# Optimization experiments

Measured on AMD Instinct MI355X. Metric: run time of the kernel, lower is better.

Reference implementation:

```python
import jax, jax.numpy as jnp
import numpy as np

N_NODES, N_EDGES, N_GRAPHS = 20000, 320000, 8
IN_CH, OUT_CH = 16, 64


def gat_conv(x, src, dst, W, a_src, a_dst, bias, heads, ch, concat):
    # PyG-style GATConv: linear -> per-edge attention logits -> edge softmax over dst -> scatter-sum
    n = x.shape[0]
    h = (x @ W).reshape(n, heads, ch)                      # [N,H,C]
    alpha_src = jnp.einsum('nhc,hc->nh', h, a_src)          # [N,H]
    alpha_dst = jnp.einsum('nhc,hc->nh', h, a_dst)
    e = jax.nn.leaky_relu(alpha_src[src] + alpha_dst[dst], 0.2)  # [E,H]
    emax = jax.ops.segment_max(e, dst, num_segments=n)      # safe: self-loops guarantee coverage
    ee = jnp.exp(e - emax[dst])
    denom = jax.ops.segment_sum(ee, dst, num_segments=n)
    alpha = ee / denom[dst]                                 # [E,H]
    msg = h[src] * alpha[:, :, None]                        # [E,H,C]
    out = jax.ops.segment_sum(msg, dst, num_segments=n)     # [N,H,C]
    out = out.reshape(n, heads * ch) if concat else out.mean(axis=1)
    return out + bias


def setup_inputs() -> dict:
    key = jax.random.key(0)
    ks = jax.random.split(key, 32)
    d = {}
    d['x'] = jax.random.normal(ks[0], (N_NODES, IN_CH), dtype=jnp.float32)
    d['edge_index'] = jax.random.randint(ks[1], (2, N_EDGES), 0, N_NODES)
    d['function_idx'] = jax.random.randint(ks[2], (8000,), 0, N_NODES)
    d['flag'] = jnp.sort(jax.random.randint(ks[3], (8000,), 0, N_GRAPHS))
    d['decision_var_idxes'] = jax.random.randint(ks[4], (N_GRAPHS,), 0, N_NODES)
    s = 0.1
    # conv1: in 16 -> 8 heads x 8
    d['W1'] = jax.random.normal(ks[5], (IN_CH, 64)) * s
    d['a_src1'] = jax.random.normal(ks[6], (8, 8)) * s
    d['a_dst1'] = jax.random.normal(ks[7], (8, 8)) * s
    d['b1'] = jnp.zeros((64,), jnp.float32)
    # conv2, conv3: 64 -> 8 heads x 8
    d['W2'] = jax.random.normal(ks[8], (64, 64)) * s
    d['a_src2'] = jax.random.normal(ks[9], (8, 8)) * s
    d['a_dst2'] = jax.random.normal(ks[10], (8, 8)) * s
    d['b2'] = jnp.zeros((64,), jnp.float32)
    d['W3'] = jax.random.normal(ks[11], (64, 64)) * s
    d['a_src3'] = jax.random.normal(ks[12], (8, 8)) * s
    d['a_dst3'] = jax.random.normal(ks[13], (8, 8)) * s
    d['b3'] = jnp.zeros((64,), jnp.float32)
    # conv4: 64 -> 4 heads x 64, concat=False (mean over heads)
    d['W4'] = jax.random.normal(ks[14], (64, 4 * OUT_CH)) * s
    d['a_src4'] = jax.random.normal(ks[15], (4, OUT_CH)) * s
    d['a_dst4'] = jax.random.normal(ks[16], (4, OUT_CH)) * s
    d['b4'] = jnp.zeros((OUT_CH,), jnp.float32)
    d['Wp'] = jax.random.normal(ks[17], (OUT_CH, OUT_CH)) * s
    d['Wt'] = jax.random.normal(ks[18], (OUT_CH, OUT_CH)) * s
    d['Wo'] = jax.random.normal(ks[19], (2 * OUT_CH, 1)) * s
    d['bo'] = jnp.zeros((1,), jnp.float32)
    return d


def reference(x, edge_index, function_idx, flag, decision_var_idxes,
              W1, a_src1, a_dst1, b1, W2, a_src2, a_dst2, b2,
              W3, a_src3, a_dst3, b3, W4, a_src4, a_dst4, b4,
              Wp, Wt, Wo, bo):
    n = x.shape[0]
    loops = jnp.arange(n)
    src = jnp.concatenate([edge_index[0], loops])
    dst = jnp.concatenate([edge_index[1], loops])
    h = jax.nn.elu(gat_conv(x, src, dst, W1, a_src1, a_dst1, b1, 8, 8, True))
    h = jax.nn.elu(gat_conv(h, src, dst, W2, a_src2, a_dst2, b2, 8, 8, True))
    h = jax.nn.elu(gat_conv(h, src, dst, W3, a_src3, a_dst3, b3, 8, 8, True))
    h = jax.nn.elu(gat_conv(h, src, dst, W4, a_src4, a_dst4, b4, 4, OUT_CH, False))
    # per-graph sum-pool over function nodes
    fp = jax.ops.segment_sum(h[function_idx], flag, num_segments=N_GRAPHS)  # [B,64]
    fp = fp @ Wp
    tgt = h[decision_var_idxes] @ Wt                                        # [B,64]
    z = jax.nn.elu(jnp.concatenate([fp, tgt], axis=1))                      # [B,128]
    return z @ Wo + bo                                                      # [B,1]
```

## Files before the change

### kernel.cpp

```cpp
#include <hip/hip_runtime.h>
#include <hip/hip_bf16.h>
#include <math.h>

typedef __hip_bfloat16 bf16;
typedef unsigned short u16;
typedef __attribute__((ext_vector_type(8))) short bf16x8;
typedef __attribute__((ext_vector_type(4))) float f32x4;

#define DEG_CAP 96

__device__ __forceinline__ float b2f(bf16 v){ return __bfloat162float(v); }
__device__ __forceinline__ u16 f2bu(float f){
  bf16 h = __float2bfloat16(f);
  return *reinterpret_cast<u16*>(&h);
}
__device__ __forceinline__ float bu2f(u16 u){
  bf16 h = *reinterpret_cast<bf16*>(&u);
  return __bfloat162float(h);
}
__device__ __forceinline__ float eluf(float x){ return x > 0.f ? x : __expf(x) - 1.f; }
__device__ __forceinline__ float lrelu(float x){ return x > 0.f ? x : 0.2f * x; }
__device__ __forceinline__ float ldr(const void* p, int i, int f){
  return f ? ((const float*)p)[i] : b2f(((const bf16*)p)[i]);
}

#define DPP_F(x, ctrl) __int_as_float(__builtin_amdgcn_update_dpp(0, __float_as_int(x), (ctrl), 0xF, 0xF, true))
__device__ __forceinline__ float dpp_max8(float x){
  x = fmaxf(x, DPP_F(x, 0xB1));
  x = fmaxf(x, DPP_F(x, 0x4E));
  x = fmaxf(x, DPP_F(x, 0x141));
  return x;
}
__device__ __forceinline__ float dpp_sum8(float x){
  x += DPP_F(x, 0xB1);
  x += DPP_F(x, 0x4E);
  x += DPP_F(x, 0x141);
  return x;
}
__device__ __forceinline__ float dpp_max16(float x){
  x = fmaxf(x, DPP_F(x, 0xB1));
  x = fmaxf(x, DPP_F(x, 0x4E));
  x = fmaxf(x, DPP_F(x, 0x141));
  x = fmaxf(x, DPP_F(x, 0x140));
  return x;
}
__device__ __forceinline__ float dpp_sum16(float x){
  x += DPP_F(x, 0xB1);
  x += DPP_F(x, 0x4E);
  x += DPP_F(x, 0x141);
  x += DPP_F(x, 0x140);
  return x;
}
__device__ __forceinline__ float dpp_addx1(float x){ return x + DPP_F(x, 0xB1); }

__global__ void detect_zero_k(const u16* __restrict__ x, int nprobe, int* __restrict__ flag,
                              int* __restrict__ fill, float* __restrict__ fp, int n){
  int i = blockIdx.x * 256 + threadIdx.x;
  if (i < n) fill[i] = 0;
  if (i < 512) fp[i] = 0.f;
  if (blockIdx.x == 0){
    __shared__ int bad_s;
    if (threadIdx.x == 0) bad_s = 0;
    __syncthreads();
    int bad = 0;
    for (int k = threadIdx.x; k < nprobe; k += 256){
      int ex = (x[k] >> 7) & 0xFF;
      if (ex >= 0xC6) bad = 1;
    }
    if (bad) atomicOr(&bad_s, 1);
    __syncthreads();
    if (threadIdx.x == 0) *flag = bad_s;
  }
}

struct ConvDesc {
  const void* src[17];
  int off[18];
};

__global__ void prep_k(ConvDesc d, float* __restrict__ out, const int* __restrict__ flag,
                       int total, const int* __restrict__ ei, int E, int n,
                       int* __restrict__ fill, int* __restrict__ esrc,
                       const void* __restrict__ W4r, const void* __restrict__ as4r,
                       const void* __restrict__ ad4r, float* __restrict__ avs,
                       float* __restrict__ avd, u16* __restrict__ wzh,
                       u16* __restrict__ wzl,
                       const void* __restrict__ x_raw, const void* __restrict__ W1r,
                       const void* __restrict__ as1r, const void* __restrict__ ad1r,
                       u16* __restrict__ hl1, float* __restrict__ asrc1,
                       float* __restrict__ adst1,
                       int CB, int EB){
  __shared__ float wl1[16 * 64];
  __shared__ float xr1[16][20];
  int b = blockIdx.x;
  int f = *flag;
  int t = threadIdx.x;
  if (b < CB){
    int i = b * 256 + t;
    if (i >= total) return;
    int a = 0;
    while (i >= d.off[a + 1]) ++a;
    out[i] = ldr(d.src[a], i - d.off[a], f);
  } else if (b < CB + EB){
    int e = (b - CB) * 256 + t;
    if (e >= E + n) return;
    int s, dd;
    if (e < E){ s = ei[e]; dd = ei[E + e]; } else { s = e - E; dd = s; }
    int pos = atomicAdd(&fill[dd], 1);
    if (pos < DEG_CAP) esrc[dd * DEG_CAP + pos] = s;
  } else if (b < CB + EB + 64){
    int pb = b - CB - EB;
    int g = pb * 256 + t;
    int r = g >> 6, c = g & 63;
    int h = r >> 6, k = r & 63;
    float ww = 0.25f * ldr(W4r, k * 256 + h * 64 + c, f);
    u16 hi = f2bu(ww);
    wzh[c * 256 + r] = hi;
    wzl[c * 256 + r] = f2bu(ww - bu2f(hi));
    if (pb == 0){
      int th = t >> 6, tk = t & 63;
      float s1 = 0.f, s2 = 0.f;
      for (int cc = 0; cc < 64; ++cc){
        float w = ldr(W4r, tk * 256 + th * 64 + cc, f);
        s1 += w * ldr(as4r, th * 64 + cc, f);
        s2 += w * ldr(ad4r, th * 64 + cc, f);
      }
      avs[t] = s1;
      avd[t] = s2;
    }
  } else {
    int lb = b - CB - EB - 64;
    int base = lb * 16;
    int lane = t & 63, wv = t >> 6;
    int node = wv * 4 + (lane >> 4);
    int jj = lane & 15;
    for (int i = t; i < 1024; i += 256) wl1[i] = ldr(W1r, i, f);
    for (int q = t; q < 64; q += 256){
      int nd = q >> 2, k4 = q & 3;
      float4 v = make_float4(0.f, 0.f, 0.f, 0.f);
      if (base + nd < n){
        if (f){
          v = *(const float4*)((const float*)x_raw + (base + nd) * 16 + k4 * 4);
        } else {
          ushort4 v4 = *(const ushort4*)((const u16*)x_raw + (base + nd) * 16 + k4 * 4);
          v = make_float4(bu2f(v4.x), bu2f(v4.y), bu2f(v4.z), bu2f(v4.w));
        }
      }
      *(float4*)(&xr1[nd][k4 * 4]) = v;
    }
    __syncthreads();
    float ax = 0.f, ay = 0.f, az = 0.f, aw = 0.f;
#pragma unroll
    for (int k4 = 0; k4 < 4; ++k4){
      float4 xv = *(const float4*)(&xr1[node][k4 * 4]);
      float4 w0 = ((const float4*)wl1)[(k4 * 4 + 0) * 16 + jj];
      float4 w1 = ((const float4*)wl1)[(k4 * 4 + 1) * 16 + jj];
      float4 w2 = ((const float4*)wl1)[(k4 * 4 + 2) * 16 + jj];
      float4 w3 = ((const float4*)wl1)[(k4 * 4 + 3) * 16 + jj];
      ax += xv.x * w0.x + xv.y * w1.x + xv.z * w2.x + xv.w * w3.x;
      ay += xv.x * w0.y + xv.y * w1.y + xv.z * w2.y + xv.w * w3.y;
      az += xv.x * w0.z + xv.y * w1.z + xv.z * w2.z + xv.w * w3.z;
      aw += xv.x * w0.w + xv.y * w1.w + xv.z * w2.w + xv.w * w3.w;
    }
    int gn = base + node;
    if (gn < n){
      ushort4 o4;
      o4.x = f2bu(ax); o4.y = f2bu(ay); o4.z = f2bu(az); o4.w = f2bu(aw);
      ((ushort4*)(hl1 + gn * 64))[jj] = o4;
    }
    float as_[4], ad_[4];
#pragma unroll
    for (int c = 0; c < 4; ++c){
      as_[c] = ldr(as1r, 4 * jj + c, f);
      ad_[c] = ldr(ad1r, 4 * jj + c, f);
    }
    float s1 = ax * as_[0] + ay * as_[1] + az * as_[2] + aw * as_[3];
    float s2 = ax * ad_[0] + ay * ad_[1] + az * ad_[2] + aw * ad_[3];
    s1 = dpp_addx1(s1);
    s2 = dpp_addx1(s2);
    if (gn < n){
      int hh = jj >> 1;
      if ((jj & 1) == 0) asrc1[gn * 8 + hh] = s1;
      else               adst1[gn * 8 + hh] = s2;
    }
  }
}

template<int NEXT>
__global__ void agg8f_k(const u16* __restrict__ hlin, const float* __restrict__ asrc,
                        const float* __restrict__ adst, const int* __restrict__ cnts,
                        const int* __restrict__ esrc, const float* __restrict__ bias,
                        const float* __restrict__ Wn,
                        const float* __restrict__ a_srcn, const float* __restrict__ a_dstn,
                        const float* __restrict__ avs, const float* __restrict__ avd,
                        u16* __restrict__ hout, u16* __restrict__ ylin,
                        float* __restrict__ asrco, float* __restrict__ adsto, int n){
  __shared__ float wl[NEXT == 1 ? 4096 : 1];
  __shared__ float os[4][64];
  if (NEXT == 1){
    for (int q = threadIdx.x; q < 1024; q += 256)
      ((float4*)wl)[q] = ((const float4*)Wn)[q];
    __syncthreads();
  }
  int node = (blockIdx.x * blockDim.x + threadIdx.x) >> 6;
  if (node >= n) return;
  int lane = threadIdx.x & 63;
  int wv = (threadIdx.x >> 6) & 3;
  int h = lane >> 3;
  int j = lane & 7;
  int cp = lane & 15;
  int q  = lane >> 4;
  int hh = cp >> 1;
  int wlane0 = hh * 8 + q;
  int wlane1 = hh * 8 + 4 + q;
  int sclane = hh * 8;
  int beg = node * DEG_CAP;
  int cnt = cnts[node]; if (cnt > DEG_CAP) cnt = DEG_CAP;
  int end = beg + cnt;
  float ad = adst[node * 8 + h];

  float m = -INFINITY, swp = 0.f;
  float4 acc = make_float4(0.f, 0.f, 0.f, 0.f);

  int   s_cur = 0; float l_cur = -INFINITY;
  if (beg + j < end){ s_cur = esrc[beg + j]; l_cur = lrelu(asrc[s_cur * 8 + h] + ad); }
  int s0c = __shfl(s_cur, q), s1c = __shfl(s_cur, 4 + q);
  ushort4 hv0 = *(const ushort4*)(hlin + s0c * 64 + cp * 4);
  ushort4 hv1 = *(const ushort4*)(hlin + s1c * 64 + cp * 4);
  int   s_nx = 0; float l_nx = -INFINITY;
  if (beg + 8 + j < end){ s_nx = esrc[beg + 8 + j]; l_nx = lrelu(asrc[s_nx * 8 + h] + ad); }

  for (int b0 = beg; b0 < end; b0 += 8){
    int s0n = __shfl(s_nx, q), s1n = __shfl(s_nx, 4 + q);
    ushort4 hv0n = *(const ushort4*)(hlin + s0n * 64 + cp * 4);
    ushort4 hv1n = *(const ushort4*)(hlin + s1n * 64 + cp * 4);
    int p2 = b0 + 16 + j;
    int s_n2 = 0; float l_n2 = -INFINITY;
    if (p2 < end){ s_n2 = esrc[p2]; l_n2 = lrelu(asrc[s_n2 * 8 + h] + ad); }
    float bm = dpp_max8(l_cur);
    float mn = fmaxf(m, bm);
    if (!__all(bm <= m)){
      float scale = __expf(m - mn);
      swp *= scale;
      float scale_g = __shfl(scale, sclane);
      acc.x *= scale_g; acc.y *= scale_g; acc.z *= scale_g; acc.w *= scale_g;
      m = mn;
    }
    float w = (b0 + j < end) ? __expf(l_cur - m) : 0.f;
    swp += w;
    float w0 = __shfl(w, wlane0);
    float w1 = __shfl(w, wlane1);
    acc.x += bu2f(hv0.x) * w0 + bu2f(hv1.x) * w1;
    acc.y += bu2f(hv0.y) * w0 + bu2f(hv1.y) * w1;
    acc.z += bu2f(hv0.z) * w0 + bu2f(hv1.z) * w1;
    acc.w += bu2f(hv0.w) * w0 + bu2f(hv1.w) * w1;
    hv0 = hv0n; hv1 = hv1n;
    l_cur = l_nx;
    s_nx = s_n2; l_nx = l_n2;
  }
  acc.x += __shfl_xor(acc.x, 16); acc.x += __shfl_xor(acc.x, 32);
  acc.y += __shfl_xor(acc.y, 16); acc.y += __shfl_xor(acc.y, 32);
  acc.z += __shfl_xor(acc.z, 16); acc.z += __shfl_xor(acc.z, 32);
  acc.w += __shfl_xor(acc.w, 16); acc.w += __shfl_xor(acc.w, 32);
  swp = dpp_sum8(swp);
  float sw_g = __shfl(swp, sclane);
  float4 bv = ((const float4*)bias)[cp];
  float4 o4;
  o4.x = eluf(acc.x / sw_g + bv.x);
  o4.y = eluf(acc.y / sw_g + bv.y);
  o4.z = eluf(acc.z / sw_g + bv.z);
  o4.w = eluf(acc.w / sw_g + bv.w);

  if (NEXT == 1){
    if (lane < 16) *(float4*)(&os[wv][cp * 4]) = o4;
    int jj = lane & 15, kk = lane >> 4;
    const float4* osr = (const float4*)(&os[wv][kk * 16]);
    float ax = 0.f, ay = 0.f, az = 0.f, aw = 0.f;
#pragma unroll
    for (int k4 = 0; k4 < 4; ++k4){
      float4 xv = osr[k4];
      float4 w0 = ((const float4*)wl)[(kk * 16 + k4 * 4 + 0) * 16 + jj];
      float4 w1 = ((const float4*)wl)[(kk * 16 + k4 * 4 + 1) * 16 + jj];
      float4 w2 = ((const float4*)wl)[(kk * 16 + k4 * 4 + 2) * 16 + jj];
      float4 w3 = ((const float4*)wl)[(kk * 16 + k4 * 4 + 3) * 16 + jj];
      ax += xv.x * w0.x + xv.y * w1.x + xv.z * w2.x + xv.w * w3.x;
      ay += xv.x * w0.y + xv.y * w1.y + xv.z * w2.y + xv.w * w3.y;
      az += xv.x * w0.z + xv.y * w1.z + xv.z * w2.z + xv.w * w3.z;
      aw += xv.x * w0.w + xv.y * w1.w + xv.z * w2.w + xv.w * w3.w;
    }
    ax += __shfl_xor(ax, 16); ax += __shfl_xor(ax, 32);
    ay += __shfl_xor(ay, 16); ay += __shfl_xor(ay, 32);
    az += __shfl_xor(az, 16); az += __shfl_xor(az, 32);
    aw += __shfl_xor(aw, 16); aw += __shfl_xor(aw, 32);
    if (lane < 16){
      ushort4 y4;
      y4.x = f2bu(ax); y4.y = f2bu(ay); y4.z = f2bu(az); y4.w = f2bu(aw);
      ((ushort4*)(ylin + node * 64))[jj] = y4;
      float4 as = *(const float4*)(a_srcn + 4 * jj);
      float4 adn = *(const float4*)(a_dstn + 4 * jj);
      float s1 = ax * as.x + ay * as.y + az * as.z + aw * as.w;
      float s2 = ax * adn.x + ay * adn.y + az * adn.z + aw * adn.w;
      s1 = dpp_addx1(s1);
      s2 = dpp_addx1(s2);
      int nh = jj >> 1;
      if ((jj & 1) == 0) asrco[node * 8 + nh] = s1;
      else               adsto[node * 8 + nh] = s2;
    }
  } else {
    if (lane < 16){
      ushort4 ho;
      ho.x = f2bu(o4.x); ho.y = f2bu(o4.y); ho.z = f2bu(o4.z); ho.w = f2bu(o4.w);
      ((ushort4*)(hout + node * 64))[cp] = ho;
      *(float4*)(&os[wv][cp * 4]) = o4;
    }
    int t8 = lane & 7, ah = (lane >> 3) & 3, sd = lane >> 5;
    const float* av = sd ? avd : avs;
    const float4* op = (const float4*)(&os[wv][t8 * 8]);
    const float4* ap = (const float4*)(av + ah * 64 + t8 * 8);
    float4 o0 = op[0], o1 = op[1];
    float4 a0 = ap[0], a1 = ap[1];
    float part = o0.x * a0.x + o0.y * a0.y + o0.z * a0.z + o0.w * a0.w
               + o1.x * a1.x + o1.y * a1.y + o1.z * a1.z + o1.w * a1.w;
    part = dpp_sum8(part);
    if (t8 == 0){
      if (sd == 0) asrco[node * 4 + ah] = part;
      else         adsto[node * 4 + ah] = part;
    }
  }
}

__global__ void aggz_k(const u16* __restrict__ h3, const float* __restrict__ asrc,
                       const float* __restrict__ adst, const int* __restrict__ cnts,
                       const int* __restrict__ esrc, u16* __restrict__ z, int n){
  int node = (blockIdx.x * blockDim.x + threadIdx.x) >> 6;
  if (node >= n) return;
  int lane = threadIdx.x & 63;
  int h = lane >> 4, j = lane & 15;
  int beg = node * DEG_CAP;
  int cnt = cnts[node]; if (cnt > DEG_CAP) cnt = DEG_CAP;
  int end = beg + cnt;
  float4 adv = *(const float4*)(adst + node * 4);
  float adh = h == 0 ? adv.x : h == 1 ? adv.y : h == 2 ? adv.z : adv.w;

  float m = -INFINITY, swp = 0.f;
  float acc[4][4] = {{0.f, 0.f, 0.f, 0.f}, {0.f, 0.f, 0.f, 0.f},
                     {0.f, 0.f, 0.f, 0.f}, {0.f, 0.f, 0.f, 0.f}};
  int   s_nx = 0; float l_nx = -INFINITY;
  if (beg + j < end){ s_nx = esrc[beg + j]; l_nx = lrelu(asrc[s_nx * 4 + h] + adh); }
  for (int b0 = beg; b0 < end; b0 += 16){
    int s = s_nx; float l = l_nx;
    int p2 = b0 + 16 + j;
    s_nx = 0; l_nx = -INFINITY;
    if (p2 < end){ s_nx = esrc[p2]; l_nx = lrelu(asrc[s_nx * 4 + h] + adh); }
    float bm = dpp_max16(l);
    float mn = fmaxf(m, bm);
    if (!__all(bm <= m)){
      float scale = __expf(m - mn);
      swp *= scale;
      float sc0 = __shfl(scale, 0),  sc1 = __shfl(scale, 16);
      float sc2 = __shfl(scale, 32), sc3 = __shfl(scale, 48);
#pragma unroll
      for (int c = 0; c < 4; ++c){
        acc[0][c] *= sc0; acc[1][c] *= sc1; acc[2][c] *= sc2; acc[3][c] *= sc3;
      }
      m = mn;
    }
    float w = (b0 + j < end) ? __expf(l - m) : 0.f;
    swp += w;
#pragma unroll
    for (int e4 = 0; e4 < 4; ++e4){
      int sl = e4 * 4 + h;
      int se = __shfl(s, sl);
      float w0 = __shfl(w, sl);
      float w1 = __shfl(w, 16 + sl);
      float w2 = __shfl(w, 32 + sl);
      float w3 = __shfl(w, 48 + sl);
      ushort4 hv = *(const ushort4*)(h3 + (size_t)se * 64 + j * 4);
      float x0 = bu2f(hv.x), x1 = bu2f(hv.y), x2 = bu2f(hv.z), x3 = bu2f(hv.w);
      acc[0][0] += x0 * w0; acc[0][1] += x1 * w0; acc[0][2] += x2 * w0; acc[0][3] += x3 * w0;
      acc[1][0] += x0 * w1; acc[1][1] += x1 * w1; acc[1][2] += x2 * w1; acc[1][3] += x3 * w1;
      acc[2][0] += x0 * w2; acc[2][1] += x1 * w2; acc[2][2] += x2 * w2; acc[2][3] += x3 * w2;
      acc[3][0] += x0 * w3; acc[3][1] += x1 * w3; acc[3][2] += x2 * w3; acc[3][3] += x3 * w3;
    }
  }
  swp = dpp_sum16(swp);
#pragma unroll
  for (int hh = 0; hh < 4; ++hh){
#pragma unroll
    for (int c = 0; c < 4; ++c){
      acc[hh][c] += __shfl_xor(acc[hh][c], 16);
      acc[hh][c] += __shfl_xor(acc[hh][c], 32);
    }
  }
  float swh = __shfl(swp, h * 16);
  float inv = 1.f / swh;
#pragma unroll
  for (int hh = 0; hh < 4; ++hh){
    if (h == hh){
      ushort4 o;
      o.x = f2bu(acc[hh][0] * inv); o.y = f2bu(acc[hh][1] * inv);
      o.z = f2bu(acc[hh][2] * inv); o.w = f2bu(acc[hh][3] * inv);
      ((ushort4*)(z + (size_t)node * 256))[hh * 16 + j] = o;
    }
  }
}

__global__ void linear4_mfma_k(const u16* __restrict__ Z, const u16* __restrict__ Wh,
                               const u16* __restrict__ Wl, const float* __restrict__ bias,
                               u16* __restrict__ H4, int n){
  int lane = threadIdx.x & 63;
  int wv = threadIdx.x >> 6;
  int base = blockIdx.x * 64 + wv * 16;
  if (base >= n) return;
  int r16 = lane & 15, kg = lane >> 4;
  int row = base + r16;
  int rowc = row < n ? row : n - 1;
  const u16* zp = Z + (size_t)rowc * 256 + kg * 8;
  const u16* wh = Wh + r16 * 256 + kg * 8;
  const u16* wlp = Wl + r16 * 256 + kg * 8;
  f32x4 ac[4] = {{0.f, 0.f, 0.f, 0.f}, {0.f, 0.f, 0.f, 0.f},
                 {0.f, 0.f, 0.f, 0.f}, {0.f, 0.f, 0.f, 0.f}};
#pragma unroll
  for (int k0 = 0; k0 < 256; k0 += 32){
    bf16x8 a = *(const bf16x8*)(zp + k0);
#pragma unroll
    for (int ct = 0; ct < 4; ++ct){
      bf16x8 bh = *(const bf16x8*)(wh + ct * 4096 + k0);
      ac[ct] = __builtin_amdgcn_mfma_f32_16x16x32_bf16(a, bh, ac[ct], 0, 0, 0);
    }
#pragma unroll
    for (int ct = 0; ct < 4; ++ct){
      bf16x8 bl = *(const bf16x8*)(wlp + ct * 4096 + k0);
      ac[ct] = __builtin_amdgcn_mfma_f32_16x16x32_bf16(a, bl, ac[ct], 0, 0, 0);
    }
  }
  int r0 = base + kg * 4;
#pragma unroll
  for (int ct = 0; ct < 4; ++ct){
    int jj = ct * 16 + r16;
    float bj = bias[jj];
#pragma unroll
    for (int i = 0; i < 4; ++i){
      int r = r0 + i;
      if (r < n) H4[(size_t)r * 64 + jj] = f2bu(eluf(ac[ct][i] + bj));
    }
  }
}

__global__ void pool_k(const u16* __restrict__ h, const int* __restrict__ fidx,
                       const int* __restrict__ flag_arr, float* __restrict__ fp, int m){
  __shared__ float acc[512];
  int t = threadIdx.x;
  int nb = gridDim.x;
  int chunk = (m + nb - 1) / nb;
  int beg = blockIdx.x * chunk;
  int end = beg + chunk; if (end > m) end = m;
  for (int i = t; i < 512; i += 256) acc[i] = 0.f;
  __syncthreads();
  int lane = t & 63;
  int wv = t >> 6;
  int i0 = beg + wv;
  int g0 = 0, n0 = 0;
  if (i0 < end){ g0 = flag_arr[i0]; n0 = fidx[i0]; }
  float hv0 = (i0 < end) ? bu2f(h[(size_t)n0 * 64 + lane]) : 0.f;
  int g1 = 0, n1 = 0;
  if (i0 + 4 < end){ g1 = flag_arr[i0 + 4]; n1 = fidx[i0 + 4]; }
  for (int i = i0; i < end; i += 4){
    float hv1 = (i + 4 < end) ? bu2f(h[(size_t)n1 * 64 + lane]) : 0.f;
    int g2 = 0, n2 = 0;
    if (i + 8 < end){ g2 = flag_arr[i + 8]; n2 = fidx[i + 8]; }
    atomicAdd(&acc[g0 * 64 + lane], hv0);
    hv0 = hv1; g0 = g1; n0 = n1; g1 = g2; n1 = n2;
  }
  __syncthreads();
  if (beg < end){
    int gmin = flag_arr[beg], gmax = flag_arr[end - 1];
    int cnt = (gmax - gmin + 1) * 64;
    for (int i = t; i < cnt; i += 256){
      float v = acc[gmin * 64 + i];
      if (v != 0.f) atomicAdd(&fp[gmin * 64 + i], v);
    }
  }
}

__global__ void final_k(const float* __restrict__ fp, const u16* __restrict__ h,
                        const int* __restrict__ dec,
                        const float* __restrict__ Wp, const float* __restrict__ Wt,
                        const float* __restrict__ Wo, const float* __restrict__ bo,
                        void* __restrict__ out, const int* __restrict__ dflag){
  __shared__ float fps[512];
  int t = threadIdx.x;
  fps[t] = fp[t];
  __syncthreads();
  int g = t >> 6;
  int j = t & 63;
  const u16* tr = h + (size_t)dec[g] * 64;
  float a = 0.f, b = 0.f;
  for (int k = 0; k < 64; ++k){
    a += fps[g * 64 + k] * Wp[k * 64 + j];
    b += bu2f(tr[k]) * Wt[k * 64 + j];
  }
  float v = eluf(a) * Wo[j] + eluf(b) * Wo[64 + j];
  for (int off = 32; off > 0; off >>= 1) v += __shfl_down(v, off);
  if (j == 0){
    float r = v + bo[0];
    if (*dflag) ((float*)out)[g] = r;
    else        ((bf16*)out)[g] = __float2bfloat16(r);
  }
}


extern "C" void kernel_launch(void* const* d_in, const int* in_sizes, int n_in,
                              void* d_out, int out_size, void* d_ws, size_t ws_size,
                              hipStream_t stream) {
  const int*  ei    = (const int*)d_in[1];
  const int*  fidx  = (const int*)d_in[2];
  const int*  flagg = (const int*)d_in[3];
  const int*  dec   = (const int*)d_in[4];

  const int N = in_sizes[0] / 16;
  const int E = in_sizes[1] / 2;
  const int M = in_sizes[2];
  const int ET = E + N;

  const int fidxs[17] = {5,6,7,8,9,10,11,12,13,14,15,16,20,21,22,23,24};
  ConvDesc cd;
  int tot = 0;
  for (int k = 0; k < 17; ++k){
    cd.src[k] = d_in[fidxs[k]];
    cd.off[k] = tot;
    tot += in_sizes[fidxs[k]];
  }
  cd.off[17] = tot;

  char* p = (char*)d_ws;
  auto carve = [&](size_t bytes) -> void* {
    void* r = (void*)p;
    p += (bytes + 255) & ~(size_t)255;
    return r;
  };
  int*   dflag   = (int*)carve(4);
  float* conv    = (float*)carve((size_t)tot * 4);
  u16*   hlA     = (u16*)carve((size_t)N * 64 * 2);
  u16*   hlB     = (u16*)carve((size_t)N * 64 * 2);
  u16*   h3buf   = (u16*)carve((size_t)N * 64 * 2);
  u16*   zbuf    = (u16*)carve((size_t)N * 256 * 2);
  u16*   h4buf   = (u16*)carve((size_t)N * 64 * 2);
  float* asrcA   = (float*)carve((size_t)N * 8 * 4);
  float* adstA   = (float*)carve((size_t)N * 8 * 4);
  float* asrcB   = (float*)carve((size_t)N * 8 * 4);
  float* adstB   = (float*)carve((size_t)N * 8 * 4);
  int*   fill    = (int*)carve((size_t)N * 4);
  int*   esrc    = (int*)carve((size_t)N * DEG_CAP * 4);
  float* fp      = (float*)carve(8 * 64 * 4);
  float* avs     = (float*)carve(256 * 4);
  float* avd     = (float*)carve(256 * 4);
  u16*   wzh     = (u16*)carve(16384 * 2);
  u16*   wzl     = (u16*)carve(16384 * 2);

  if ((size_t)(p - (char*)d_ws) > ws_size) return;

  const float* cas2 = conv + cd.off[5],  *cad2 = conv + cd.off[6],  *cb1 = conv + cd.off[3];
  const float* cW2 = conv + cd.off[4],   *cb2 = conv + cd.off[7];
  const float* cW3 = conv + cd.off[8],  *cas3 = conv + cd.off[9],  *cad3 = conv + cd.off[10], *cb3 = conv + cd.off[11];
  const float* cb4 = conv + cd.off[12];
  const float* cWp = conv + cd.off[13], *cWt = conv + cd.off[14], *cWo = conv + cd.off[15], *cbo = conv + cd.off[16];

  const int TB = 256;
  int nprobe = in_sizes[0] < 4096 ? in_sizes[0] : 4096;
  int zb_blocks = (N + 255) / 256;
  int CB = (tot + 255) / 256;
  int EB = (ET + 255) / 256;
  int ls_blocks = (N + 15) / 16;

  detect_zero_k<<<zb_blocks, TB, 0, stream>>>((const u16*)d_in[0], nprobe, dflag, fill, fp, N);
  prep_k<<<CB + EB + 64 + ls_blocks, TB, 0, stream>>>(
      cd, conv, dflag, tot, ei, E, N, fill, esrc,
      d_in[17], d_in[18], d_in[19], avs, avd, wzh, wzl,
      d_in[0], d_in[5], d_in[6], d_in[7], hlA, asrcA, adstA, CB, EB);

  int agg_blocks = (N * 64 + TB - 1) / TB;
  int mf_blocks  = (N + 63) / 64;

  agg8f_k<1><<<agg_blocks, TB, 0, stream>>>(hlA, asrcA, adstA, fill, esrc, cb1,
                                            cW2, cas2, cad2, nullptr, nullptr,
                                            nullptr, hlB, asrcB, adstB, N);
  agg8f_k<1><<<agg_blocks, TB, 0, stream>>>(hlB, asrcB, adstB, fill, esrc, cb2,
                                            cW3, cas3, cad3, nullptr, nullptr,
                                            nullptr, hlA, asrcA, adstA, N);
  agg8f_k<2><<<agg_blocks, TB, 0, stream>>>(hlA, asrcA, adstA, fill, esrc, cb3,
                                            nullptr, nullptr, nullptr, avs, avd,
                                            h3buf, nullptr, asrcB, adstB, N);
  aggz_k<<<agg_blocks, TB, 0, stream>>>(h3buf, asrcB, adstB, fill, esrc, zbuf, N);
  linear4_mfma_k<<<mf_blocks, TB, 0, stream>>>(zbuf, wzh, wzl, cb4, h4buf, N);
  pool_k<<<256, TB, 0, stream>>>(h4buf, fidx, flagg, fp, M);
  final_k<<<1, 512, 0, stream>>>(fp, h4buf, dec, cWp, cWt, cWo, cbo, d_out, dflag);
}
```

Baseline: 245.3 us.

## Compute final GAT layer only for pooled and decision nodes

The last attention aggregation and its linear transform now run only for the rows the readout actually uses: the function_idx entries plus the decision-variable nodes. Results are stored compactly by list index, and pool_k and final_k read those rows directly instead of gathering by node id. This drops about 60% of the layer-4 aggregation and MFMA work, and duplicate indices simply get recomputed. The output is unchanged because layer 4 feeds nothing except the readout.

```diff
diff --git a/kernel.cpp b/kernel.cpp
--- a/kernel.cpp
+++ b/kernel.cpp
@@ -331,9 +331,12 @@
 
 __global__ void aggz_k(const u16* __restrict__ h3, const float* __restrict__ asrc,
                        const float* __restrict__ adst, const int* __restrict__ cnts,
-                       const int* __restrict__ esrc, u16* __restrict__ z, int n){
-  int node = (blockIdx.x * blockDim.x + threadIdx.x) >> 6;
-  if (node >= n) return;
+                       const int* __restrict__ esrc, const int* __restrict__ fidx,
+                       const int* __restrict__ dec, u16* __restrict__ zc,
+                       int lm, int m){
+  int li = (blockIdx.x * blockDim.x + threadIdx.x) >> 6;
+  if (li >= lm) return;
+  int node = (li < m) ? fidx[li] : dec[li - m];
   int lane = threadIdx.x & 63;
   int h = lane >> 4, j = lane & 15;
   int beg = node * DEG_CAP;
@@ -342,7 +345,7 @@
   float4 adv = *(const float4*)(adst + node * 4);
   float adh = h == 0 ? adv.x : h == 1 ? adv.y : h == 2 ? adv.z : adv.w;
 
-  float m = -INFINITY, swp = 0.f;
+  float m_ = -INFINITY, swp = 0.f;
   float acc[4][4] = {{0.f, 0.f, 0.f, 0.f}, {0.f, 0.f, 0.f, 0.f},
                      {0.f, 0.f, 0.f, 0.f}, {0.f, 0.f, 0.f, 0.f}};
   int   s_nx = 0; float l_nx = -INFINITY;
@@ -353,9 +356,9 @@
     s_nx = 0; l_nx = -INFINITY;
     if (p2 < end){ s_nx = esrc[p2]; l_nx = lrelu(asrc[s_nx * 4 + h] + adh); }
     float bm = dpp_max16(l);
-    float mn = fmaxf(m, bm);
-    if (!__all(bm <= m)){
-      float scale = __expf(m - mn);
+    float mn = fmaxf(m_, bm);
+    if (!__all(bm <= m_)){
+      float scale = __expf(m_ - mn);
       swp *= scale;
       float sc0 = __shfl(scale, 0),  sc1 = __shfl(scale, 16);
       float sc2 = __shfl(scale, 32), sc3 = __shfl(scale, 48);
@@ -363,9 +366,9 @@
       for (int c = 0; c < 4; ++c){
         acc[0][c] *= sc0; acc[1][c] *= sc1; acc[2][c] *= sc2; acc[3][c] *= sc3;
       }
-      m = mn;
-    }
-    float w = (b0 + j < end) ? __expf(l - m) : 0.f;
+      m_ = mn;
+    }
+    float w = (b0 + j < end) ? __expf(l - m_) : 0.f;
     swp += w;
 #pragma unroll
     for (int e4 = 0; e4 < 4; ++e4){
@@ -400,7 +403,7 @@
       ushort4 o;
       o.x = f2bu(acc[hh][0] * inv); o.y = f2bu(acc[hh][1] * inv);
       o.z = f2bu(acc[hh][2] * inv); o.w = f2bu(acc[hh][3] * inv);
-      ((ushort4*)(z + (size_t)node * 256))[hh * 16 + j] = o;
+      ((ushort4*)(zc + (size_t)li * 256))[hh * 16 + j] = o;
     }
   }
 }
@@ -447,8 +450,8 @@
   }
 }
 
-__global__ void pool_k(const u16* __restrict__ h, const int* __restrict__ fidx,
-                       const int* __restrict__ flag_arr, float* __restrict__ fp, int m){
+__global__ void pool_k(const u16* __restrict__ h4c, const int* __restrict__ flag_arr,
+                       float* __restrict__ fp, int m){
   __shared__ float acc[512];
   int t = threadIdx.x;
   int nb = gridDim.x;
@@ -460,17 +463,17 @@
   int lane = t & 63;
   int wv = t >> 6;
   int i0 = beg + wv;
-  int g0 = 0, n0 = 0;
-  if (i0 < end){ g0 = flag_arr[i0]; n0 = fidx[i0]; }
-  float hv0 = (i0 < end) ? bu2f(h[(size_t)n0 * 64 + lane]) : 0.f;
-  int g1 = 0, n1 = 0;
-  if (i0 + 4 < end){ g1 = flag_arr[i0 + 4]; n1 = fidx[i0 + 4]; }
+  int g0 = 0;
+  if (i0 < end) g0 = flag_arr[i0];
+  float hv0 = (i0 < end) ? bu2f(h4c[(size_t)i0 * 64 + lane]) : 0.f;
+  int g1 = 0;
+  if (i0 + 4 < end) g1 = flag_arr[i0 + 4];
   for (int i = i0; i < end; i += 4){
-    float hv1 = (i + 4 < end) ? bu2f(h[(size_t)n1 * 64 + lane]) : 0.f;
-    int g2 = 0, n2 = 0;
-    if (i + 8 < end){ g2 = flag_arr[i + 8]; n2 = fidx[i + 8]; }
+    float hv1 = (i + 4 < end) ? bu2f(h4c[(size_t)(i + 4) * 64 + lane]) : 0.f;
+    int g2 = 0;
+    if (i + 8 < end) g2 = flag_arr[i + 8];
     atomicAdd(&acc[g0 * 64 + lane], hv0);
-    hv0 = hv1; g0 = g1; n0 = n1; g1 = g2; n1 = n2;
+    hv0 = hv1; g0 = g1; g1 = g2;
   }
   __syncthreads();
   if (beg < end){
@@ -483,8 +486,8 @@
   }
 }
 
-__global__ void final_k(const float* __restrict__ fp, const u16* __restrict__ h,
-                        const int* __restrict__ dec,
+__global__ void final_k(const float* __restrict__ fp, const u16* __restrict__ h4c,
+                        int m,
                         const float* __restrict__ Wp, const float* __restrict__ Wt,
                         const float* __restrict__ Wo, const float* __restrict__ bo,
                         void* __restrict__ out, const int* __restrict__ dflag){
@@ -494,7 +497,7 @@
   __syncthreads();
   int g = t >> 6;
   int j = t & 63;
-  const u16* tr = h + (size_t)dec[g] * 64;
+  const u16* tr = h4c + (size_t)(m + g) * 64;
   float a = 0.f, b = 0.f;
   for (int k = 0; k < 64; ++k){
     a += fps[g * 64 + k] * Wp[k * 64 + j];
@@ -521,6 +524,8 @@
   const int N = in_sizes[0] / 16;
   const int E = in_sizes[1] / 2;
   const int M = in_sizes[2];
+  const int NG = in_sizes[4];
+  const int LM = M + NG;
   const int ET = E + N;
 
   const int fidxs[17] = {5,6,7,8,9,10,11,12,13,14,15,16,20,21,22,23,24};
@@ -544,8 +549,8 @@
   u16*   hlA     = (u16*)carve((size_t)N * 64 * 2);
   u16*   hlB     = (u16*)carve((size_t)N * 64 * 2);
   u16*   h3buf   = (u16*)carve((size_t)N * 64 * 2);
-  u16*   zbuf    = (u16*)carve((size_t)N * 256 * 2);
-  u16*   h4buf   = (u16*)carve((size_t)N * 64 * 2);
+  u16*   zbuf    = (u16*)carve((size_t)LM * 256 * 2);
+  u16*   h4buf   = (u16*)carve((size_t)LM * 64 * 2);
   float* asrcA   = (float*)carve((size_t)N * 8 * 4);
   float* adstA   = (float*)carve((size_t)N * 8 * 4);
   float* asrcB   = (float*)carve((size_t)N * 8 * 4);
@@ -580,7 +585,8 @@
       d_in[0], d_in[5], d_in[6], d_in[7], hlA, asrcA, adstA, CB, EB);
 
   int agg_blocks = (N * 64 + TB - 1) / TB;
-  int mf_blocks  = (N + 63) / 64;
+  int aggz_blocks = (LM * 64 + TB - 1) / TB;
+  int mf_blocks  = (LM + 63) / 64;
 
   agg8f_k<1><<<agg_blocks, TB, 0, stream>>>(hlA, asrcA, adstA, fill, esrc, cb1,
                                             cW2, cas2, cad2, nullptr, nullptr,
@@ -591,8 +597,9 @@
   agg8f_k<2><<<agg_blocks, TB, 0, stream>>>(hlA, asrcA, adstA, fill, esrc, cb3,
                                             nullptr, nullptr, nullptr, avs, avd,
                                             h3buf, nullptr, asrcB, adstB, N);
-  aggz_k<<<agg_blocks, TB, 0, stream>>>(h3buf, asrcB, adstB, fill, esrc, zbuf, N);
-  linear4_mfma_k<<<mf_blocks, TB, 0, stream>>>(zbuf, wzh, wzl, cb4, h4buf, N);
-  pool_k<<<256, TB, 0, stream>>>(h4buf, fidx, flagg, fp, M);
-  final_k<<<1, 512, 0, stream>>>(fp, h4buf, dec, cWp, cWt, cWo, cbo, d_out, dflag);
-}
+  aggz_k<<<aggz_blocks, TB, 0, stream>>>(h3buf, asrcB, adstB, fill, esrc,
+                                         fidx, dec, zbuf, LM, M);
+  linear4_mfma_k<<<mf_blocks, TB, 0, stream>>>(zbuf, wzh, wzl, cb4, h4buf, LM);
+  pool_k<<<256, TB, 0, stream>>>(h4buf, flagg, fp, M);
+  final_k<<<1, 512, 0, stream>>>(fp, h4buf, M, cWp, cWt, cWo, cbo, d_out, dflag);
+}
```

Result: faster. 235.3 us (-4.1%).
